# Kernel tuning notes

Hardware: AMD Instinct MI355X
Metric: run time of the kernel (lower is better)

Reference implementation:

```python
import jax, jax.numpy as jnp
import numpy as np
import math

B, L = 4, 2048
D_MODEL, N_HEADS, D_K, D_V, D_FF, FACTOR = 512, 8, 64, 64, 2048, 5


def _layernorm(x, g, b, eps=1e-5):
    m = x.mean(-1, keepdims=True)
    v = jnp.mean((x - m) ** 2, axis=-1, keepdims=True)
    return (x - m) * jax.lax.rsqrt(v + eps) * g + b


def setup_inputs() -> dict:
    key = jax.random.key(0)
    ks = jax.random.split(key, 8)
    w = lambda k, shape: (jax.random.normal(k, shape, jnp.float32) * 0.02)
    sample_k = min(FACTOR * int(math.ceil(math.log(L))), L)  # c*ln(L_K) sampled keys per query
    return {
        "x": jax.random.normal(ks[0], (B, L, D_MODEL), jnp.float32),
        "Wq": w(ks[1], (D_MODEL, N_HEADS * D_K)),
        "Wk": w(ks[2], (D_MODEL, N_HEADS * D_K)),
        "Wv": w(ks[3], (D_MODEL, N_HEADS * D_V)),
        "Wo": w(ks[4], (N_HEADS * D_V, D_MODEL)),
        "ln1_g": jnp.ones((D_MODEL,), jnp.float32),
        "ln1_b": jnp.zeros((D_MODEL,), jnp.float32),
        "conv1_w": w(ks[5], (D_FF, D_MODEL)),
        "conv1_b": jnp.zeros((D_FF,), jnp.float32),
        "conv2_w": w(ks[6], (D_MODEL, D_FF)),
        "conv2_b": jnp.zeros((D_MODEL,), jnp.float32),
        "ln2_g": jnp.ones((D_MODEL,), jnp.float32),
        "ln2_b": jnp.zeros((D_MODEL,), jnp.float32),
        # Informer samples sample_k random keys per query position (constant indices)
        "sample_idx": jax.random.randint(ks[7], (L, sample_k), 0, L),
    }


def reference(x, Wq, Wk, Wv, Wo, ln1_g, ln1_b, conv1_w, conv1_b, conv2_w, conv2_b, ln2_g, ln2_b, sample_idx):
    Bx, Lx, D = x.shape
    H = N_HEADS
    # projections -> [B,H,L,d]
    Q = (x @ Wq).reshape(Bx, Lx, H, D_K).transpose(0, 2, 1, 3)
    K = (x @ Wk).reshape(Bx, Lx, H, D_K).transpose(0, 2, 1, 3)
    V = (x @ Wv).reshape(Bx, Lx, H, D_V).transpose(0, 2, 1, 3)

    u = min(FACTOR * int(math.ceil(math.log(Lx))), Lx)  # top-u active queries
    # sampled QK scores: [B,H,L,sample_k]
    K_samp = K[:, :, sample_idx]                              # [B,H,L,S,dk]
    qk_s = jnp.einsum('bhle,bhlse->bhls', Q, K_samp)
    # sparsity measure M = max - mean (Informer divides sum by L_K)
    M = qk_s.max(-1) - qk_s.sum(-1) / Lx                      # [B,H,L]
    _, top = jax.lax.top_k(M, u)                              # [B,H,u]

    Q_red = jnp.take_along_axis(Q, top[..., None], axis=2)    # [B,H,u,dk]
    scores = jnp.einsum('bhue,bhle->bhul', Q_red, K) / math.sqrt(D_K)
    attn = jax.nn.softmax(scores, axis=-1)                    # [B,H,u,L]

    # initial context = mean of V over keys; update only top-u query rows
    ctx = jnp.broadcast_to(V.mean(axis=2, keepdims=True), V.shape)  # [B,H,L,dv]
    upd = jnp.einsum('bhul,bhld->bhud', attn, V)              # [B,H,u,dv]
    bi = jnp.arange(Bx)[:, None, None]
    hi = jnp.arange(H)[None, :, None]
    ctx = ctx.at[bi, hi, top].set(upd)

    out = ctx.transpose(0, 2, 1, 3).reshape(Bx, Lx, H * D_V) @ Wo
    x1 = _layernorm(x + out, ln1_g, ln1_b)  # residual + norm inside attention sublayer

    # conv1d(k=1) FFN == per-token linear; dropout is identity in eval
    y = jax.nn.gelu(x1 @ conv1_w.T + conv1_b, approximate=False)
    y = y @ conv2_w.T + conv2_b
    return _layernorm(x1 + y, ln2_g, ln2_b)
```

## Files before the change

kernel.cpp:

```cpp
#include <hip/hip_runtime.h>
#include <hip/hip_bf16.h>

#define BB 4
#define LL 2048
#define DD 512
#define HH 8
#define DKK 64
#define FF 2048

typedef __bf16  bf16x8  __attribute__((ext_vector_type(8)));
typedef float   floatx4 __attribute__((ext_vector_type(4)));

__device__ __forceinline__ void async_cp16(const void* g, void* l) {
    __builtin_amdgcn_global_load_lds(
        (const __attribute__((address_space(1))) unsigned int*)g,
        (__attribute__((address_space(3))) unsigned int*)l,
        16, 0, 0);
}

__device__ __forceinline__ float gelu_f(float v) {
    float z  = v * 0.70710678118654752f;
    float az = fabsf(z);
    float t  = __builtin_amdgcn_rcpf(1.0f + 0.3275911f * az);
    float p  = ((((1.061405429f * t - 1.453152027f) * t + 1.421413741f) * t
                 - 0.284496736f) * t + 0.254829592f) * t;
    float e  = __expf(-z * z);
    float er = 1.0f - p * e;
    er = (z < 0.0f) ? -er : er;
    return 0.5f * v * (1.0f + er);
}

__global__ __launch_bounds__(256) void prep_w(
    const float* __restrict__ Wq, const float* __restrict__ Wk,
    const float* __restrict__ Wv, const float* __restrict__ Wo,
    __bf16* __restrict__ wb)
{
    const size_t SZ = (size_t)DD * DD;
    int z = blockIdx.z;
    const float* s = (z == 0) ? Wq : (z == 1) ? Wk : (z == 2) ? Wv : Wo;
    __bf16* hi; __bf16* lo = nullptr;
    if (z == 0)      { hi = wb;          lo = wb + SZ; }
    else if (z == 1) { hi = wb + 2 * SZ; lo = wb + 3 * SZ; }
    else if (z == 2) { hi = wb + 4 * SZ; }
    else             { hi = wb + 5 * SZ; }
    int idx = blockIdx.x * 256 + threadIdx.x;
    int k = idx >> 9, n = idx & 511;
    float v = s[idx];
    __bf16 h = (__bf16)v;
    hi[(size_t)n * DD + k] = h;
    if (lo) lo[(size_t)n * DD + k] = (__bf16)(v - (float)h);
}

__global__ __launch_bounds__(256) void cast_cw(
    const float* __restrict__ c1w, const float* __restrict__ c2w,
    __bf16* __restrict__ d1, __bf16* __restrict__ d2)
{
    const float* s = blockIdx.z ? c2w : c1w;
    __bf16* d = blockIdx.z ? d2 : d1;
    int idx = blockIdx.x * 256 + threadIdx.x;
    d[idx] = (__bf16)s[idx];
}

__global__ __launch_bounds__(256) void split_cast_x(
    const float* __restrict__ x, __bf16* __restrict__ xhi, __bf16* __restrict__ xlo)
{
    int idx = blockIdx.x * 256 + threadIdx.x;
    float v = x[idx];
    __bf16 h = (__bf16)v;
    xhi[idx] = h;
    xlo[idx] = (__bf16)(v - (float)h);
}

template<int ACT, bool BIAS, bool OUT_BF16>
__global__ __launch_bounds__(256) void gemm_mfma(
    const __bf16* __restrict__ A, const __bf16* __restrict__ B,
    const float* __restrict__ bias, void* __restrict__ Cv,
    int M, int N, int K)
{
    __shared__ __bf16 As[2][128 * 32];
    __shared__ __bf16 Bs[2][128 * 32];
    const int tid = threadIdx.x;
    const int wave = tid >> 6, lane = tid & 63;
    const int gx = gridDim.x;
    const int nwg = gx * gridDim.y;
    const int hw = blockIdx.y * gx + blockIdx.x;
    const int virt = ((nwg & 7) == 0) ? ((hw & 7) * (nwg >> 3) + (hw >> 3)) : hw;
    const int m0 = (virt / gx) * 128, n0 = (virt % gx) * 128;
    const int wm = (wave >> 1) * 64, wn = (wave & 1) * 64;
    const int l15 = lane & 15, kq = lane >> 4;

    auto stage = [&](int buf, int k0) {
        #pragma unroll
        for (int p = 0; p < 2; p++) {
            int c = p * 256 + tid;
            int row = c >> 2, col = (c & 3) * 8;
            async_cp16(A + (size_t)(m0 + row) * K + k0 + col, &As[buf][c * 8]);
            async_cp16(B + (size_t)(n0 + row) * K + k0 + col, &Bs[buf][c * 8]);
        }
    };

    floatx4 acc[4][4] = {};

    stage(0, 0);
    __syncthreads();
    int cur = 0;
    for (int k0 = 0; k0 < K; k0 += 32) {
        if (k0 + 32 < K) stage(cur ^ 1, k0 + 32);
        bf16x8 af[4], bfr[4];
        #pragma unroll
        for (int i = 0; i < 4; i++)
            af[i] = *(const bf16x8*)(&As[cur][(wm + i * 16 + l15) * 32 + kq * 8]);
        #pragma unroll
        for (int j = 0; j < 4; j++)
            bfr[j] = *(const bf16x8*)(&Bs[cur][(wn + j * 16 + l15) * 32 + kq * 8]);
        #pragma unroll
        for (int i = 0; i < 4; i++)
            #pragma unroll
            for (int j = 0; j < 4; j++)
                acc[i][j] = __builtin_amdgcn_mfma_f32_16x16x32_bf16(bfr[j], af[i], acc[i][j], 0, 0, 0);
        __syncthreads();
        cur ^= 1;
    }
    #pragma unroll
    for (int i = 0; i < 4; i++) {
        int m = m0 + wm + i * 16 + l15;
        #pragma unroll
        for (int j = 0; j < 4; j++) {
            int n = n0 + wn + j * 16 + kq * 4;
            floatx4 v4 = acc[i][j];
            if (BIAS) {
                float4 bv = *(const float4*)&bias[n];
                v4[0] += bv.x; v4[1] += bv.y; v4[2] += bv.z; v4[3] += bv.w;
            }
            if (ACT == 1) {
                v4[0] = gelu_f(v4[0]); v4[1] = gelu_f(v4[1]);
                v4[2] = gelu_f(v4[2]); v4[3] = gelu_f(v4[3]);
            }
            if (OUT_BF16) {
                union { __bf16 b[4]; uint2 u; } pk;
                pk.b[0] = (__bf16)v4[0]; pk.b[1] = (__bf16)v4[1];
                pk.b[2] = (__bf16)v4[2]; pk.b[3] = (__bf16)v4[3];
                *(uint2*)((__bf16*)Cv + (size_t)m * N + n) = pk.u;
            } else {
                *(float4*)((float*)Cv + (size_t)m * N + n) = *(float4*)&v4;
            }
        }
    }
}

__global__ __launch_bounds__(256) void gemm_mfma_split(
    const __bf16* __restrict__ Ah, const __bf16* __restrict__ Al,
    const __bf16* __restrict__ Bh, const __bf16* __restrict__ Bl,
    float* __restrict__ C, int M, int N, int K)
{
    __shared__ __bf16 Ahs[2][128 * 32];
    __shared__ __bf16 Als[2][128 * 32];
    __shared__ __bf16 Bhs[2][128 * 32];
    __shared__ __bf16 Bls[2][128 * 32];
    const int tid = threadIdx.x;
    const int wave = tid >> 6, lane = tid & 63;
    const int gx = gridDim.x;
    const int nwg = gx * gridDim.y;
    const int hw = blockIdx.y * gx + blockIdx.x;
    const int virt = ((nwg & 7) == 0) ? ((hw & 7) * (nwg >> 3) + (hw >> 3)) : hw;
    const int m0 = (virt / gx) * 128, n0 = (virt % gx) * 128;
    const int wm = (wave >> 1) * 64, wn = (wave & 1) * 64;
    const int l15 = lane & 15, kq = lane >> 4;

    auto stage = [&](int buf, int k0) {
        #pragma unroll
        for (int p = 0; p < 2; p++) {
            int c = p * 256 + tid;
            int row = c >> 2, col = (c & 3) * 8;
            size_t goA = (size_t)(m0 + row) * K + k0 + col;
            size_t goB = (size_t)(n0 + row) * K + k0 + col;
            async_cp16(Ah + goA, &Ahs[buf][c * 8]);
            async_cp16(Al + goA, &Als[buf][c * 8]);
            async_cp16(Bh + goB, &Bhs[buf][c * 8]);
            async_cp16(Bl + goB, &Bls[buf][c * 8]);
        }
    };

    floatx4 acc[4][4] = {};

    stage(0, 0);
    __syncthreads();
    int cur = 0;
    for (int k0 = 0; k0 < K; k0 += 32) {
        if (k0 + 32 < K) stage(cur ^ 1, k0 + 32);
        bf16x8 ah[4], al[4], bh[4], bl[4];
        #pragma unroll
        for (int i = 0; i < 4; i++) {
            int off = (wm + i * 16 + l15) * 32 + kq * 8;
            ah[i] = *(const bf16x8*)(&Ahs[cur][off]);
            al[i] = *(const bf16x8*)(&Als[cur][off]);
        }
        #pragma unroll
        for (int j = 0; j < 4; j++) {
            int off = (wn + j * 16 + l15) * 32 + kq * 8;
            bh[j] = *(const bf16x8*)(&Bhs[cur][off]);
            bl[j] = *(const bf16x8*)(&Bls[cur][off]);
        }
        #pragma unroll
        for (int i = 0; i < 4; i++)
            #pragma unroll
            for (int j = 0; j < 4; j++) {
                acc[i][j] = __builtin_amdgcn_mfma_f32_16x16x32_bf16(bh[j], ah[i], acc[i][j], 0, 0, 0);
                acc[i][j] = __builtin_amdgcn_mfma_f32_16x16x32_bf16(bl[j], ah[i], acc[i][j], 0, 0, 0);
                acc[i][j] = __builtin_amdgcn_mfma_f32_16x16x32_bf16(bh[j], al[i], acc[i][j], 0, 0, 0);
            }
        __syncthreads();
        cur ^= 1;
    }
    #pragma unroll
    for (int i = 0; i < 4; i++) {
        int m = m0 + wm + i * 16 + l15;
        #pragma unroll
        for (int j = 0; j < 4; j++) {
            int n = n0 + wn + j * 16 + kq * 4;
            *(float4*)(C + (size_t)m * N + n) = *(float4*)&acc[i][j];
        }
    }
}

__device__ __forceinline__ float dpp_sum16(float p) {
    int t;
    t = __builtin_amdgcn_update_dpp(0, __float_as_int(p), 0xB1,  0xF, 0xF, true);
    p += __int_as_float(t);
    t = __builtin_amdgcn_update_dpp(0, __float_as_int(p), 0x4E,  0xF, 0xF, true);
    p += __int_as_float(t);
    t = __builtin_amdgcn_update_dpp(0, __float_as_int(p), 0x141, 0xF, 0xF, true);
    p += __int_as_float(t);
    t = __builtin_amdgcn_update_dpp(0, __float_as_int(p), 0x140, 0xF, 0xF, true);
    p += __int_as_float(t);
    return p;
}

__global__ __launch_bounds__(256) void calc_m(
    const float* __restrict__ Q, const float* __restrict__ Kb,
    const int* __restrict__ sidx, float* __restrict__ Mo, int U)
{
    __shared__ int   js[64];
    __shared__ float red_mx[2][HH];
    __shared__ float red_sm[2][HH];
    int i = blockIdx.x;
    int b = i & 3, l = i >> 2;
    int tid = threadIdx.x;
    if (tid < U) js[tid] = sidx[l * U + tid];
    int e    = (tid & 127) * 4;
    int slot = tid >> 7;
    const float* qr = Q + ((size_t)(b * LL + l) * DD);
    float4 q = *(const float4*)(qr + e);
    const float* kbase = Kb + ((size_t)b * LL) * DD + e;
    __syncthreads();
    float mx = -1e30f, sm = 0.f;
    for (int s = slot; s < U; s += 2) {
        int j = js[s];
        float4 kv = *(const float4*)(kbase + (size_t)j * DD);
        float p = q.x * kv.x + q.y * kv.y + q.z * kv.z + q.w * kv.w;
        p = dpp_sum16(p);
        mx = fmaxf(mx, p);
        sm += p;
    }
    if ((tid & 15) == 0) {
        int head = (tid >> 4) & 7;
        red_mx[slot][head] = mx;
        red_sm[slot][head] = sm;
    }
    __syncthreads();
    if (tid < HH) {
        float m2 = fmaxf(red_mx[0][tid], red_mx[1][tid]);
        float s2 = red_sm[0][tid] + red_sm[1][tid];
        Mo[((size_t)(b * HH + tid)) * LL + l] = m2 - s2 * (1.0f / (float)LL);
    }
}

__global__ __launch_bounds__(256) void topk_k(
    const float* __restrict__ Mo, int* __restrict__ top, int U)
{
    __shared__ unsigned int hist[256];
    __shared__ unsigned int wsum[4];
    __shared__ unsigned int bc[2];
    __shared__ int ties[LL];
    __shared__ int cnt2[2];
    int bh = blockIdx.x, tid = threadIdx.x;
    int lane = tid & 63, w = tid >> 6;

    unsigned int my[8];
    #pragma unroll
    for (int i = 0; i < 8; i++) {
        unsigned int u = __float_as_uint(Mo[(size_t)bh * LL + tid + i * 256]);
        my[i] = u ^ ((u >> 31) ? 0xFFFFFFFFu : 0x80000000u);
    }

    unsigned int prefix = 0, pmask = 0;
    unsigned int need = (unsigned int)U;
    unsigned int above = 0;

    for (int pass = 0; pass < 4; pass++) {
        int shift = 24 - pass * 8;
        hist[tid] = 0;
        __syncthreads();
        #pragma unroll
        for (int i = 0; i < 8; i++) {
            unsigned int u = my[i];
            if ((u & pmask) == prefix)
                atomicAdd(&hist[(u >> shift) & 255u], 1u);
        }
        __syncthreads();
        unsigned int h = hist[tid];
        #pragma unroll
        for (int off = 1; off < 64; off <<= 1) {
            unsigned int o = __shfl_down(h, off);
            if (lane + off < 64) h += o;
        }
        if (lane == 0) wsum[w] = h;
        __syncthreads();
        unsigned int tail = 0;
        #pragma unroll
        for (int w2 = 1; w2 < 4; w2++) if (w2 > w) tail += wsum[w2];
        h += tail;
        hist[tid] = h;
        __syncthreads();
        unsigned int St = h;
        unsigned int St1 = (tid < 255) ? hist[tid + 1] : 0u;
        if (St >= need && St1 < need) { bc[0] = (unsigned int)tid; bc[1] = St1; }
        __syncthreads();
        unsigned int dig = bc[0], abv = bc[1];
        above += abv;
        need -= abv;
        prefix |= dig << shift;
        pmask |= 0xFFu << shift;
        __syncthreads();
    }

    if (tid == 0) { cnt2[0] = 0; cnt2[1] = 0; }
    __syncthreads();
    #pragma unroll
    for (int i = 0; i < 8; i++) {
        unsigned int u = my[i];
        int idx = tid + i * 256;
        if (u > prefix) {
            int pos = atomicAdd(&cnt2[0], 1);
            top[bh * U + pos] = idx;
        } else if (u == prefix) {
            int pos = atomicAdd(&cnt2[1], 1);
            ties[pos] = idx;
        }
    }
    __syncthreads();
    int tcnt = cnt2[1];
    #pragma unroll
    for (int i = 0; i < 8; i++) {
        unsigned int u = my[i];
        if (u == prefix) {
            int idx = tid + i * 256;
            int rank = 0;
            for (int j = 0; j < tcnt; j++) rank += (ties[j] < idx) ? 1 : 0;
            if (rank < (int)need) top[bh * U + (int)above + rank] = idx;
        }
    }
}

__global__ __launch_bounds__(256) void vmean_k(
    const __bf16* __restrict__ V, float* __restrict__ Vm)
{
    __shared__ float osum[4][DKK];
    int bh = blockIdx.x;
    int b = bh >> 3, h = bh & 7;
    int tid = threadIdx.x, d = tid & 63, part = tid >> 6;
    const __bf16* vp = V + ((size_t)(b * LL + part * 512) * DD + h * DKK + d);
    float s = 0.f;
    for (int i = 0; i < 512; i++) s += (float)vp[(size_t)i * DD];
    osum[part][d] = s;
    __syncthreads();
    if (tid < DKK)
        Vm[bh * DKK + tid] = (osum[0][tid] + osum[1][tid] + osum[2][tid] + osum[3][tid]) * (1.0f / (float)LL);
}

__global__ __launch_bounds__(256) void gather_qred(
    const float* __restrict__ Q, const int* __restrict__ top,
    __bf16* __restrict__ qred, int U)
{
    int bh = blockIdx.y;
    int b = bh >> 3, h = bh & 7;
    int e = blockIdx.x * 256 + threadIdx.x;
    int u = e >> 6, d = e & 63;
    float v = 0.f;
    if (u < U) {
        int l = top[bh * U + u];
        v = Q[((size_t)(b * LL + l) * DD + h * DKK) + d] * 0.125f;
    }
    qred[(size_t)bh * 48 * DKK + e] = (__bf16)v;
}

__global__ __launch_bounds__(256) void gemm_s(
    const __bf16* __restrict__ qred, const float* __restrict__ Kb,
    float* __restrict__ S)
{
    __shared__ __bf16 Qs[2 * 48 * 32];
    __shared__ __bf16 Ks[2 * 128 * 32];
    int bh = blockIdx.y, nc = blockIdx.x;
    int b = bh >> 3, h = bh & 7, l0 = nc * 128;
    int tid = threadIdx.x;
    const unsigned int* qsrc = (const unsigned int*)(qred + (size_t)bh * 48 * DKK);
    unsigned int* qdst = (unsigned int*)Qs;
    #pragma unroll
    for (int t = 0; t < 6; t++) {
        int ui = tid + t * 256;
        int u = ui >> 5, kp = ui & 31;
        int p = kp >> 4, kl2 = kp & 15;
        qdst[p * 768 + u * 16 + kl2] = qsrc[ui];
    }
    #pragma unroll
    for (int t = 0; t < 8; t++) {
        int fi = tid + t * 256;
        int row = fi >> 4, k4 = fi & 15;
        int p = k4 >> 3, kl = (k4 & 7) * 4;
        float4 kv = *(const float4*)(Kb + ((size_t)(b * LL + l0 + row) * DD + h * DKK + k4 * 4));
        __bf16* dst = Ks + p * 128 * 32 + row * 32 + kl;
        dst[0] = (__bf16)kv.x; dst[1] = (__bf16)kv.y;
        dst[2] = (__bf16)kv.z; dst[3] = (__bf16)kv.w;
    }
    __syncthreads();
    int wave = tid >> 6, lane = tid & 63, l15 = lane & 15, kq = lane >> 4;
    floatx4 acc[3][2] = {};
    #pragma unroll
    for (int p = 0; p < 2; p++) {
        bf16x8 bq[2];
        #pragma unroll
        for (int j = 0; j < 2; j++)
            bq[j] = *(const bf16x8*)(Ks + p * 4096 + (wave * 32 + j * 16 + l15) * 32 + kq * 8);
        #pragma unroll
        for (int i = 0; i < 3; i++) {
            bf16x8 aq = *(const bf16x8*)(Qs + p * 1536 + (i * 16 + l15) * 32 + kq * 8);
            #pragma unroll
            for (int j = 0; j < 2; j++)
                acc[i][j] = __builtin_amdgcn_mfma_f32_16x16x32_bf16(bq[j], aq, acc[i][j], 0, 0, 0);
        }
    }
    #pragma unroll
    for (int i = 0; i < 3; i++) {
        int row = i * 16 + l15;
        #pragma unroll
        for (int j = 0; j < 2; j++) {
            int col = l0 + wave * 32 + j * 16 + kq * 4;
            *(float4*)&S[((size_t)bh * 48 + row) * LL + col] = *(float4*)&acc[i][j];
        }
    }
}

__global__ __launch_bounds__(256) void softmax_p(float* __restrict__ S, int U)
{
    __shared__ float red[256];
    int row = blockIdx.x;
    int bh = row / U, u = row % U;
    float* sr = S + ((size_t)bh * 48 + u) * LL;
    int tid = threadIdx.x;
    float sc[8]; float mx = -1e30f;
    #pragma unroll
    for (int i = 0; i < 8; i++) { sc[i] = sr[tid + i * 256]; mx = fmaxf(mx, sc[i]); }
    red[tid] = mx; __syncthreads();
    for (int s = 128; s > 0; s >>= 1) { if (tid < s) red[tid] = fmaxf(red[tid], red[tid + s]); __syncthreads(); }
    mx = red[0]; __syncthreads();
    float se = 0.f;
    #pragma unroll
    for (int i = 0; i < 8; i++) { sc[i] = __expf(sc[i] - mx); se += sc[i]; }
    red[tid] = se; __syncthreads();
    for (int s = 128; s > 0; s >>= 1) { if (tid < s) red[tid] += red[tid + s]; __syncthreads(); }
    float inv = 1.0f / red[0];
    __bf16* pr = (__bf16*)sr;
    #pragma unroll
    for (int i = 0; i < 8; i++) pr[tid + i * 256] = (__bf16)(sc[i] * inv);
}

__global__ __launch_bounds__(256) void pv_k(
    const float* __restrict__ S, const __bf16* __restrict__ V,
    float* __restrict__ upd, int U)
{
    __shared__ __bf16 pls[4 * LL];
    __shared__ float osum[4][4][DKK];
    int bh = blockIdx.y, uc = blockIdx.x;
    int b = bh >> 3, h = bh & 7, tid = threadIdx.x;
    #pragma unroll
    for (int t = 0; t < 16; t++) {
        int ui = tid + t * 256;
        int up = ui >> 10, lw = ui & 1023;
        const unsigned int* src = (const unsigned int*)(S + ((size_t)bh * 48 + uc * 4 + up) * LL);
        ((unsigned int*)pls)[up * 1024 + lw] = src[lw];
    }
    __syncthreads();
    int d = tid & 63, part = tid >> 6;
    float a0 = 0.f, a1 = 0.f, a2 = 0.f, a3 = 0.f;
    const __bf16* vp = V + ((size_t)(b * LL + part * 512) * DD + h * DKK + d);
    int lbase = part * 512;
    for (int i = 0; i < 512; i++) {
        float v = (float)vp[(size_t)i * DD];
        int l = lbase + i;
        a0 += (float)pls[l] * v;
        a1 += (float)pls[LL + l] * v;
        a2 += (float)pls[2 * LL + l] * v;
        a3 += (float)pls[3 * LL + l] * v;
    }
    osum[part][0][d] = a0; osum[part][1][d] = a1;
    osum[part][2][d] = a2; osum[part][3][d] = a3;
    __syncthreads();
    int u2 = tid >> 6;
    float s = osum[0][u2][d] + osum[1][u2][d] + osum[2][u2][d] + osum[3][u2][d];
    upd[((size_t)bh * U + uc * 4 + u2) * DKK + d] = s;
}

__global__ __launch_bounds__(256) void ctx_init(
    const float* __restrict__ Vm, __bf16* __restrict__ ctx)
{
    int idx = blockIdx.x * 256 + threadIdx.x;
    int c = idx & 511; int h = c >> 6, d = c & 63;
    int bl = idx >> 9; int b = bl >> 11;
    ctx[idx] = (__bf16)Vm[(b * HH + h) * DKK + d];
}
__global__ __launch_bounds__(256) void ctx_scatter(
    const float* __restrict__ upd, const int* __restrict__ top,
    __bf16* __restrict__ ctx, int U, int total)
{
    int idx = blockIdx.x * 256 + threadIdx.x;
    if (idx >= total) return;
    int d = idx & 63; int ru = idx >> 6;
    int bh = ru / U, u = ru % U;
    int b = bh >> 3, h = bh & 7;
    int l = top[bh * U + u];
    ctx[(((size_t)(b * LL + l)) << 9) + h * DKK + d] = (__bf16)upd[idx];
}

__global__ __launch_bounds__(256) void ln1_k(
    const float* __restrict__ x, const float* __restrict__ aout,
    const float* __restrict__ g, const float* __restrict__ bb,
    __bf16* __restrict__ x1h)
{
    __shared__ float red[256];
    int row = blockIdx.x, tid = threadIdx.x;
    size_t base = (size_t)row * DD;
    float h0 = x[base + tid] + aout[base + tid];
    float h1 = x[base + 256 + tid] + aout[base + 256 + tid];
    red[tid] = h0 + h1; __syncthreads();
    for (int s = 128; s > 0; s >>= 1) { if (tid < s) red[tid] += red[tid + s]; __syncthreads(); }
    float mean = red[0] * (1.0f / DD); __syncthreads();
    float d0 = h0 - mean, d1 = h1 - mean;
    red[tid] = d0 * d0 + d1 * d1; __syncthreads();
    for (int s = 128; s > 0; s >>= 1) { if (tid < s) red[tid] += red[tid + s]; __syncthreads(); }
    float rstd = rsqrtf(red[0] * (1.0f / DD) + 1e-5f);
    x1h[base + tid]       = (__bf16)(d0 * rstd * g[tid] + bb[tid]);
    x1h[base + 256 + tid] = (__bf16)(d1 * rstd * g[256 + tid] + bb[256 + tid]);
}

__global__ __launch_bounds__(256) void ln2_k(
    const __bf16* __restrict__ x1h, const float* __restrict__ f2o,
    const float* __restrict__ c2b,
    const float* __restrict__ g, const float* __restrict__ bb,
    float* __restrict__ out)
{
    __shared__ float red[256];
    int row = blockIdx.x, tid = threadIdx.x;
    size_t base = (size_t)row * DD;
    float h0 = (float)x1h[base + tid] + f2o[base + tid] + c2b[tid];
    float h1 = (float)x1h[base + 256 + tid] + f2o[base + 256 + tid] + c2b[256 + tid];
    red[tid] = h0 + h1; __syncthreads();
    for (int s = 128; s > 0; s >>= 1) { if (tid < s) red[tid] += red[tid + s]; __syncthreads(); }
    float mean = red[0] * (1.0f / DD); __syncthreads();
    float d0 = h0 - mean, d1 = h1 - mean;
    red[tid] = d0 * d0 + d1 * d1; __syncthreads();
    for (int s = 128; s > 0; s >>= 1) { if (tid < s) red[tid] += red[tid + s]; __syncthreads(); }
    float rstd = rsqrtf(red[0] * (1.0f / DD) + 1e-5f);
    out[base + tid]       = d0 * rstd * g[tid] + bb[tid];
    out[base + 256 + tid] = d1 * rstd * g[256 + tid] + bb[256 + tid];
}

extern "C" void kernel_launch(void* const* d_in, const int* in_sizes, int n_in,
                              void* d_out, int out_size, void* d_ws, size_t ws_size,
                              hipStream_t stream)
{
    const float* x   = (const float*)d_in[0];
    const float* Wq  = (const float*)d_in[1];
    const float* Wk  = (const float*)d_in[2];
    const float* Wv  = (const float*)d_in[3];
    const float* Wo  = (const float*)d_in[4];
    const float* g1  = (const float*)d_in[5];
    const float* b1  = (const float*)d_in[6];
    const float* c1w = (const float*)d_in[7];
    const float* c1b = (const float*)d_in[8];
    const float* c2w = (const float*)d_in[9];
    const float* c2b = (const float*)d_in[10];
    const float* g2  = (const float*)d_in[11];
    const float* b2  = (const float*)d_in[12];
    const int* sidx  = (const int*)d_in[13];
    float* out       = (float*)d_out;

    const int U = in_sizes[13] / LL;
    const int M = BB * LL;

    char* ws = (char*)d_ws;
    const size_t MB = (size_t)1 << 20;
    float*  Q    = (float*)(ws + 0);
    float*  Kb   = (float*)(ws + 16 * MB);
    __bf16* V    = (__bf16*)(ws + 32 * MB);
    __bf16* xhi  = (__bf16*)(ws + 40 * MB);
    __bf16* xlo  = (__bf16*)(ws + 48 * MB);
    float*  S    = (float*)(ws + 40 * MB);
    __bf16* wb   = (__bf16*)(ws + 56 * MB);
    __bf16* c1wb = (__bf16*)(ws + 59 * MB);
    __bf16* c2wb = (__bf16*)(ws + 61 * MB);
    float*  Mo   = (float*)(ws + 63 * MB);
    float*  upd  = (float*)(ws + 63 * MB + 256 * 1024);
    float*  Vm   = (float*)(ws + 63 * MB + 576 * 1024);
    int*    top  = (int*)  (ws + 63 * MB + 584 * 1024);
    __bf16* qred = (__bf16*)(ws + 63 * MB + 592 * 1024);
    float*  aout = Q;
    float*  f2o  = Q;
    __bf16* ctx  = V;
    __bf16* ych  = (__bf16*)(ws + 16 * MB);
    __bf16* x1h  = xlo;
    (void)ws_size; (void)n_in; (void)out_size;

    const size_t SZ = (size_t)DD * DD;
    __bf16* WqThi = wb;          __bf16* WqTlo = wb + SZ;
    __bf16* WkThi = wb + 2 * SZ; __bf16* WkTlo = wb + 3 * SZ;
    __bf16* WvT   = wb + 4 * SZ; __bf16* WoT   = wb + 5 * SZ;

    prep_w<<<dim3(DD * DD / 256, 1, 4), 256, 0, stream>>>(Wq, Wk, Wv, Wo, wb);
    cast_cw<<<dim3(FF * DD / 256, 1, 2), 256, 0, stream>>>(c1w, c2w, c1wb, c2wb);
    split_cast_x<<<BB * LL * DD / 256, 256, 0, stream>>>(x, xhi, xlo);

    dim3 gproj(DD / 128, M / 128);
    gemm_mfma_split<<<gproj, 256, 0, stream>>>(xhi, xlo, WqThi, WqTlo, Q,  M, DD, DD);
    gemm_mfma_split<<<gproj, 256, 0, stream>>>(xhi, xlo, WkThi, WkTlo, Kb, M, DD, DD);
    gemm_mfma<0, false, true ><<<gproj, 256, 0, stream>>>(xhi, WvT, nullptr, V, M, DD, DD);

    calc_m<<<BB * LL, 256, 0, stream>>>(Q, Kb, sidx, Mo, U);
    topk_k<<<BB * HH, 256, 0, stream>>>(Mo, top, U);
    vmean_k<<<BB * HH, 256, 0, stream>>>(V, Vm);

    gather_qred<<<dim3(48 * DKK / 256, BB * HH), 256, 0, stream>>>(Q, top, qred, U);
    gemm_s<<<dim3(LL / 128, BB * HH), 256, 0, stream>>>(qred, Kb, S);
    softmax_p<<<BB * HH * U, 256, 0, stream>>>(S, U);
    pv_k<<<dim3(U / 4, BB * HH), 256, 0, stream>>>(S, V, upd, U);

    ctx_init<<<M * DD / 256, 256, 0, stream>>>(Vm, ctx);
    int sc_total = BB * HH * U * DKK;
    ctx_scatter<<<(sc_total + 255) / 256, 256, 0, stream>>>(upd, top, ctx, U, sc_total);
    gemm_mfma<0, false, false><<<gproj, 256, 0, stream>>>(ctx, WoT, nullptr, aout, M, DD, DD);

    ln1_k<<<M, 256, 0, stream>>>(x, aout, g1, b1, x1h);

    gemm_mfma<1, true,  true ><<<dim3(FF / 128, M / 128), 256, 0, stream>>>(x1h, c1wb, c1b, ych, M, FF, DD);
    gemm_mfma<0, false, false><<<dim3(DD / 128, M / 128), 256, 0, stream>>>(ych, c2wb, nullptr, f2o, M, DD, FF);

    ln2_k<<<M, 256, 0, stream>>>(x1h, f2o, c2b, g2, b2, out);
}
```

Measured before the change: 421.2 us.

## Triple-buffer GEMM LDS staging with explicit vmcnt waits for deeper prefetch

Both MFMA GEMM kernels move from double-buffered to triple-buffered LDS staging. Each iteration prefetches the tile two steps ahead and waits with a partial s_waitcnt vmcnt, which lets the newest loads stay in flight. Raw s_barrier calls replace __syncthreads, so the global-to-LDS load latency is hidden over two compute steps. In exchange the kernels use 50% more LDS, which can reduce occupancy; the split kernel rises to 96KB. Correctness now depends on the hand-set vmcnt counts matching the number of async loads per stage.

Result: no change. 414.8 us (-1.5%).

```diff
diff --git a/kernel.cpp b/kernel.cpp
--- a/kernel.cpp
+++ b/kernel.cpp
@@ -77,8 +77,8 @@
     const float* __restrict__ bias, void* __restrict__ Cv,
     int M, int N, int K)
 {
-    __shared__ __bf16 As[2][128 * 32];
-    __shared__ __bf16 Bs[2][128 * 32];
+    __shared__ __bf16 As[3][128 * 32];
+    __shared__ __bf16 Bs[3][128 * 32];
     const int tid = threadIdx.x;
     const int wave = tid >> 6, lane = tid & 63;
     const int gx = gridDim.x;
@@ -101,25 +101,38 @@
 
     floatx4 acc[4][4] = {};
 
+    const int nt = K >> 5;
     stage(0, 0);
-    __syncthreads();
-    int cur = 0;
-    for (int k0 = 0; k0 < K; k0 += 32) {
-        if (k0 + 32 < K) stage(cur ^ 1, k0 + 32);
+    stage(1, 32);
+    int bi = 0;
+    for (int t = 0; t < nt; t++) {
+        int k2 = (t + 2) << 5;
+        if (k2 < K) {
+            int b2 = bi + 2; if (b2 >= 3) b2 -= 3;
+            stage(b2, k2);
+            asm volatile("s_waitcnt vmcnt(8)" ::: "memory");
+        } else if (t + 1 < nt) {
+            asm volatile("s_waitcnt vmcnt(4)" ::: "memory");
+        } else {
+            asm volatile("s_waitcnt vmcnt(0)" ::: "memory");
+        }
+        __builtin_amdgcn_s_barrier();
+        asm volatile("" ::: "memory");
         bf16x8 af[4], bfr[4];
         #pragma unroll
         for (int i = 0; i < 4; i++)
-            af[i] = *(const bf16x8*)(&As[cur][(wm + i * 16 + l15) * 32 + kq * 8]);
+            af[i] = *(const bf16x8*)(&As[bi][(wm + i * 16 + l15) * 32 + kq * 8]);
         #pragma unroll
         for (int j = 0; j < 4; j++)
-            bfr[j] = *(const bf16x8*)(&Bs[cur][(wn + j * 16 + l15) * 32 + kq * 8]);
+            bfr[j] = *(const bf16x8*)(&Bs[bi][(wn + j * 16 + l15) * 32 + kq * 8]);
         #pragma unroll
         for (int i = 0; i < 4; i++)
             #pragma unroll
             for (int j = 0; j < 4; j++)
                 acc[i][j] = __builtin_amdgcn_mfma_f32_16x16x32_bf16(bfr[j], af[i], acc[i][j], 0, 0, 0);
-        __syncthreads();
-        cur ^= 1;
+        asm volatile("" ::: "memory");
+        __builtin_amdgcn_s_barrier();
+        if (++bi == 3) bi = 0;
     }
     #pragma unroll
     for (int i = 0; i < 4; i++) {
@@ -153,10 +166,10 @@
     const __bf16* __restrict__ Bh, const __bf16* __restrict__ Bl,
     float* __restrict__ C, int M, int N, int K)
 {
-    __shared__ __bf16 Ahs[2][128 * 32];
-    __shared__ __bf16 Als[2][128 * 32];
-    __shared__ __bf16 Bhs[2][128 * 32];
-    __shared__ __bf16 Bls[2][128 * 32];
+    __shared__ __bf16 Ahs[3][128 * 32];
+    __shared__ __bf16 Als[3][128 * 32];
+    __shared__ __bf16 Bhs[3][128 * 32];
+    __shared__ __bf16 Bls[3][128 * 32];
     const int tid = threadIdx.x;
     const int wave = tid >> 6, lane = tid & 63;
     const int gx = gridDim.x;
@@ -183,23 +196,35 @@
 
     floatx4 acc[4][4] = {};
 
+    const int nt = K >> 5;
     stage(0, 0);
-    __syncthreads();
-    int cur = 0;
-    for (int k0 = 0; k0 < K; k0 += 32) {
-        if (k0 + 32 < K) stage(cur ^ 1, k0 + 32);
+    stage(1, 32);
+    int bi = 0;
+    for (int t = 0; t < nt; t++) {
+        int k2 = (t + 2) << 5;
+        if (k2 < K) {
+            int b2 = bi + 2; if (b2 >= 3) b2 -= 3;
+            stage(b2, k2);
+            asm volatile("s_waitcnt vmcnt(16)" ::: "memory");
+        } else if (t + 1 < nt) {
+            asm volatile("s_waitcnt vmcnt(8)" ::: "memory");
+        } else {
+            asm volatile("s_waitcnt vmcnt(0)" ::: "memory");
+        }
+        __builtin_amdgcn_s_barrier();
+        asm volatile("" ::: "memory");
         bf16x8 ah[4], al[4], bh[4], bl[4];
         #pragma unroll
         for (int i = 0; i < 4; i++) {
             int off = (wm + i * 16 + l15) * 32 + kq * 8;
-            ah[i] = *(const bf16x8*)(&Ahs[cur][off]);
-            al[i] = *(const bf16x8*)(&Als[cur][off]);
+            ah[i] = *(const bf16x8*)(&Ahs[bi][off]);
+            al[i] = *(const bf16x8*)(&Als[bi][off]);
         }
         #pragma unroll
         for (int j = 0; j < 4; j++) {
             int off = (wn + j * 16 + l15) * 32 + kq * 8;
-            bh[j] = *(const bf16x8*)(&Bhs[cur][off]);
-            bl[j] = *(const bf16x8*)(&Bls[cur][off]);
+            bh[j] = *(const bf16x8*)(&Bhs[bi][off]);
+            bl[j] = *(const bf16x8*)(&Bls[bi][off]);
         }
         #pragma unroll
         for (int i = 0; i < 4; i++)
@@ -209,8 +234,9 @@
                 acc[i][j] = __builtin_amdgcn_mfma_f32_16x16x32_bf16(bl[j], ah[i], acc[i][j], 0, 0, 0);
                 acc[i][j] = __builtin_amdgcn_mfma_f32_16x16x32_bf16(bh[j], al[i], acc[i][j], 0, 0, 0);
             }
-        __syncthreads();
-        cur ^= 1;
+        asm volatile("" ::: "memory");
+        __builtin_amdgcn_s_barrier();
+        if (++bi == 3) bi = 0;
     }
     #pragma unroll
     for (int i = 0; i < 4; i++) {
```
